# Performance work log

Measured on AMD Instinct MI355X. Metric: run time of the kernel, lower is better.

The kernel has to match this reference:

```python
import jax, jax.numpy as jnp
import numpy as np
from jax import lax


def _conv2d_same(x, w):
    # x: [B,Cin,H,W], w: [Cout,Cin,kh,kw], stride 1, SAME padding
    return lax.conv_general_dilated(x, w, (1, 1), 'SAME',
                                    dimension_numbers=('NCHW', 'OIHW', 'NCHW'))


def _descriptor(f_flat, w_a, b_a, w_aa, b_aa, w_m, b_m, w_mm, b_mm):
    # f_flat: [B,C,HW]; channel MLPs on avg/max pooled descriptors (1x1 convs == linear)
    avg = jnp.mean(f_flat, axis=-1)  # [B,C]
    mx = jnp.max(f_flat, axis=-1)    # [B,C]
    a = jax.nn.relu(avg @ w_a.T + b_a) @ w_aa.T + b_aa  # [B,C]
    m = jax.nn.relu(mx @ w_m.T + b_m) @ w_mm.T + b_mm   # [B,C]
    return a + m


def _spatial_gate(a_flat, b, c, h, w, conv1_w, conv1_b, conv2_w, conv2_b):
    a = a_flat.reshape(b, c, h, w)
    pooled = jnp.stack([jnp.mean(a, axis=1), jnp.max(a, axis=1)], axis=1)  # [B,2,H,W]
    y = jax.nn.relu(_conv2d_same(pooled, conv1_w) + conv1_b[None, :, None, None])
    y = _conv2d_same(y, conv2_w) + conv2_b[None, :, None, None]
    return jax.nn.softmax(y.reshape(b, 1, h * w), axis=-1)  # [B,1,HW]


def _cafm_forward(f1, f2,
                  w_avg1, b_avg1, w_max1, b_max1, w_avg11, b_avg11, w_max11, b_max11,
                  w_avg2, b_avg2, w_max2, b_max2, w_avg22, b_avg22, w_max22, b_max22,
                  conv1_w, conv1_b, conv2_w, conv2_b):
    b, c, h, w = f1.shape
    f1f = f1.reshape(b, c, h * w)
    f2f = f2.reshape(b, c, h * w)
    a1 = _descriptor(f1f, w_avg1, b_avg1, w_avg11, b_avg11, w_max1, b_max1, w_max11, b_max11)
    a2 = _descriptor(f2f, w_avg2, b_avg2, w_avg22, b_avg22, w_max2, b_max2, w_max22, b_max22)
    cross = jnp.einsum('bi,bj->bij', a1, a2)  # [B,C,C]
    at1 = jnp.einsum('bij,bjn->bin', jax.nn.softmax(cross, axis=-1), f1f)
    at2 = jnp.einsum('bij,bjn->bin', jax.nn.softmax(cross.transpose(0, 2, 1), axis=-1), f2f)
    g1 = _spatial_gate(at1, b, c, h, w, conv1_w, conv1_b, conv2_w, conv2_b)
    g2 = _spatial_gate(at2, b, c, h, w, conv1_w, conv1_b, conv2_w, conv2_b)
    o1 = (f1f * g1 + f1f).reshape(b, c, h, w)
    o2 = (f2f * g2 + f2f).reshape(b, c, h, w)
    return o1, o2


def setup_inputs() -> dict:
    key = jax.random.key(0)
    ks = jax.random.split(key, 24)
    B, C, H, W = 4, 64, 256, 256
    CR = 32  # reduction channels
    s = 0.05
    d = {
        'f1': jax.random.normal(ks[0], (B, C, H, W), jnp.float32),
        'f2': jax.random.normal(ks[1], (B, C, H, W), jnp.float32),
        'w_avg1': jax.random.normal(ks[2], (CR, C), jnp.float32) * s,
        'b_avg1': jnp.zeros((CR,), jnp.float32),
        'w_max1': jax.random.normal(ks[3], (CR, C), jnp.float32) * s,
        'b_max1': jnp.zeros((CR,), jnp.float32),
        'w_avg11': jax.random.normal(ks[4], (C, CR), jnp.float32) * s,
        'b_avg11': jnp.zeros((C,), jnp.float32),
        'w_max11': jax.random.normal(ks[5], (C, CR), jnp.float32) * s,
        'b_max11': jnp.zeros((C,), jnp.float32),
        'w_avg2': jax.random.normal(ks[6], (CR, C), jnp.float32) * s,
        'b_avg2': jnp.zeros((CR,), jnp.float32),
        'w_max2': jax.random.normal(ks[7], (CR, C), jnp.float32) * s,
        'b_max2': jnp.zeros((CR,), jnp.float32),
        'w_avg22': jax.random.normal(ks[8], (C, CR), jnp.float32) * s,
        'b_avg22': jnp.zeros((C,), jnp.float32),
        'w_max22': jax.random.normal(ks[9], (C, CR), jnp.float32) * s,
        'b_max22': jnp.zeros((C,), jnp.float32),
        'conv1_w': jax.random.normal(ks[10], (1, 2, 3, 3), jnp.float32) * s,
        'conv1_b': jnp.zeros((1,), jnp.float32),
        'conv2_w': jax.random.normal(ks[11], (1, 1, 3, 3), jnp.float32) * s,
        'conv2_b': jnp.zeros((1,), jnp.float32),
    }
    return d


def reference(f1, f2,
              w_avg1, b_avg1, w_max1, b_max1, w_avg11, b_avg11, w_max11, b_max11,
              w_avg2, b_avg2, w_max2, b_max2, w_avg22, b_avg22, w_max22, b_max22,
              conv1_w, conv1_b, conv2_w, conv2_b):
    return _cafm_forward(f1, f2,
                         w_avg1, b_avg1, w_max1, b_max1, w_avg11, b_avg11, w_max11, b_max11,
                         w_avg2, b_avg2, w_max2, b_max2, w_avg22, b_avg22, w_max22, b_max22,
                         conv1_w, conv1_b, conv2_w, conv2_b)
```

## Files before the change

### kernel.cpp

```cpp
#include <hip/hip_runtime.h>
#include <hip/hip_bf16.h>
#include <cstdint>

#define HW 65536

typedef __attribute__((ext_vector_type(8))) short bf16x8;
typedef __attribute__((ext_vector_type(4))) float f32x4;

#define OFF_RSUM 0
#define OFF_RMAX 512
#define OFF_PB   1024
#define OFF_POOL 33792
#define OFF_BM   33792
#define OFF_BS   35840
#define OFF_T1   1082368
#define OFF_Y    1606656
#define OFF_MX   2130944
#define OFF_IZ   2130952

__global__ __launch_bounds__(512) void k_reduce(const float* __restrict__ f1,
                                                const float* __restrict__ f2,
                                                float* __restrict__ ws) {
  int s = blockIdx.x;
  int t = s >> 8;
  const float* base = (t ? f2 : f1) + ((size_t)(s & 255) << 16);
  const float4* p4 = (const float4*)base;
  int tid = threadIdx.x;
  float sum = 0.f, mx = -3.4e38f;
#pragma unroll 8
  for (int it = 0; it < 32; ++it) {
    float4 v = p4[tid + (it << 9)];
    sum += (v.x + v.y) + (v.z + v.w);
    mx = fmaxf(mx, fmaxf(fmaxf(v.x, v.y), fmaxf(v.z, v.w)));
  }
  for (int o = 32; o > 0; o >>= 1) {
    sum += __shfl_down(sum, o);
    mx = fmaxf(mx, __shfl_down(mx, o));
  }
  __shared__ float ls[8], lm[8];
  int wid = tid >> 6, lane = tid & 63;
  if (lane == 0) { ls[wid] = sum; lm[wid] = mx; }
  __syncthreads();
  if (tid == 0) {
    float S = ls[0], M = lm[0];
    for (int w = 1; w < 8; ++w) { S += ls[w]; M = fmaxf(M, lm[w]); }
    ws[OFF_RSUM + s] = S;
    ws[OFF_RMAX + s] = M;
  }
}

__global__ __launch_bounds__(64) void k_mlp(
    const float* __restrict__ wsin, __hip_bfloat16* __restrict__ Pb,
    const float* __restrict__ w_avg1, const float* __restrict__ b_avg1,
    const float* __restrict__ w_max1, const float* __restrict__ b_max1,
    const float* __restrict__ w_avg11, const float* __restrict__ b_avg11,
    const float* __restrict__ w_max11, const float* __restrict__ b_max11,
    const float* __restrict__ w_avg2, const float* __restrict__ b_avg2,
    const float* __restrict__ w_max2, const float* __restrict__ b_max2,
    const float* __restrict__ w_avg22, const float* __restrict__ b_avg22,
    const float* __restrict__ w_max22, const float* __restrict__ b_max22) {
  int b = blockIdx.x, tid = threadIdx.x;
  __shared__ float avg1[64], mx1[64], avg2[64], mx2[64];
  __shared__ float ha1[32], hm1[32], ha2[32], hm2[32];
  __shared__ float a1[64], a2[64];
  avg1[tid] = wsin[OFF_RSUM + b * 64 + tid] * (1.f / 65536.f);
  mx1[tid]  = wsin[OFF_RMAX + b * 64 + tid];
  avg2[tid] = wsin[OFF_RSUM + 256 + b * 64 + tid] * (1.f / 65536.f);
  mx2[tid]  = wsin[OFF_RMAX + 256 + b * 64 + tid];
  __syncthreads();
  if (tid < 32) {
    float s1 = b_avg1[tid], s2 = b_max1[tid], s3 = b_avg2[tid], s4 = b_max2[tid];
    for (int c = 0; c < 64; ++c) {
      s1 += w_avg1[tid * 64 + c] * avg1[c];
      s2 += w_max1[tid * 64 + c] * mx1[c];
      s3 += w_avg2[tid * 64 + c] * avg2[c];
      s4 += w_max2[tid * 64 + c] * mx2[c];
    }
    ha1[tid] = fmaxf(s1, 0.f); hm1[tid] = fmaxf(s2, 0.f);
    ha2[tid] = fmaxf(s3, 0.f); hm2[tid] = fmaxf(s4, 0.f);
  }
  __syncthreads();
  {
    float s1 = b_avg11[tid] + b_max11[tid];
    float s2 = b_avg22[tid] + b_max22[tid];
    for (int k = 0; k < 32; ++k) {
      s1 += w_avg11[tid * 32 + k] * ha1[k] + w_max11[tid * 32 + k] * hm1[k];
      s2 += w_avg22[tid * 32 + k] * ha2[k] + w_max22[tid * 32 + k] * hm2[k];
    }
    a1[tid] = s1; a2[tid] = s2;
  }
  __syncthreads();
  {
    float s = a1[tid], m = -3.4e38f;
    for (int j = 0; j < 64; ++j) m = fmaxf(m, s * a2[j]);
    float sum = 0.f;
    for (int j = 0; j < 64; ++j) sum += __expf(s * a2[j] - m);
    float inv = 1.f / sum;
    __hip_bfloat16* row = Pb + (b << 12) + (tid << 6);
    for (int j = 0; j < 64; ++j)
      row[j] = __float2bfloat16(__expf(s * a2[j] - m) * inv);
  }
  {
    float s = a2[tid], m = -3.4e38f;
    for (int j = 0; j < 64; ++j) m = fmaxf(m, s * a1[j]);
    float sum = 0.f;
    for (int j = 0; j < 64; ++j) sum += __expf(s * a1[j] - m);
    float inv = 1.f / sum;
    __hip_bfloat16* row = Pb + ((4 + b) << 12) + (tid << 6);
    for (int j = 0; j < 64; ++j)
      row[j] = __float2bfloat16(__expf(s * a1[j] - m) * inv);
  }
}

__global__ __launch_bounds__(256) void k_pool(const float* __restrict__ f1,
                                              const float* __restrict__ f2,
                                              const __hip_bfloat16* __restrict__ Pall,
                                              float* __restrict__ pool) {
  int bx = blockIdx.x;
  int slice = bx >> 8;
  int t = slice >> 2;
  const float* f = (t ? f2 : f1) + ((size_t)(slice & 3) << 22);
  const __hip_bfloat16* P = Pall + (slice << 12);
  int wave = threadIdx.x >> 6, lane = threadIdx.x & 63;
  int c = lane & 15, q = lane >> 4;
  int n0 = ((bx & 255) << 8) + (wave << 6);

  bf16x8 A[4][2];
#pragma unroll
  for (int mt = 0; mt < 4; ++mt)
#pragma unroll
    for (int s = 0; s < 2; ++s)
      A[mt][s] = *(const bf16x8*)(P + ((mt * 16 + c) << 6) + s * 32 + q * 8);

  const float* fq = f + (size_t)(q * 8) * HW + n0 + c;
  float* poolp = pool + ((size_t)slice << 17);

#pragma unroll 2
  for (int nt = 0; nt < 4; ++nt) {
    int d = nt << 4;
    float bv0[8], bv1[8];
#pragma unroll
    for (int j = 0; j < 8; ++j) {
      bv0[j] = fq[(size_t)j * HW + d];
      bv1[j] = fq[(size_t)(j + 32) * HW + d];
    }
    union { bf16x8 v; __hip_bfloat162 h[4]; } u0, u1;
#pragma unroll
    for (int jj = 0; jj < 4; ++jj) {
      u0.h[jj] = __float22bfloat162_rn(make_float2(bv0[2 * jj], bv0[2 * jj + 1]));
      u1.h[jj] = __float22bfloat162_rn(make_float2(bv1[2 * jj], bv1[2 * jj + 1]));
    }
    f32x4 acc[4];
#pragma unroll
    for (int mt = 0; mt < 4; ++mt) {
      acc[mt] = (f32x4){0.f, 0.f, 0.f, 0.f};
      acc[mt] = __builtin_amdgcn_mfma_f32_16x16x32_bf16(A[mt][0], u0.v, acc[mt], 0, 0, 0);
      acc[mt] = __builtin_amdgcn_mfma_f32_16x16x32_bf16(A[mt][1], u1.v, acc[mt], 0, 0, 0);
    }
    float sum = 0.f, mxv = -3.4e38f;
#pragma unroll
    for (int mt = 0; mt < 4; ++mt)
#pragma unroll
      for (int r = 0; r < 4; ++r) {
        float v = acc[mt][r];
        sum += v;
        mxv = fmaxf(mxv, v);
      }
    sum += __shfl_xor(sum, 16);
    sum += __shfl_xor(sum, 32);
    mxv = fmaxf(mxv, __shfl_xor(mxv, 16));
    mxv = fmaxf(mxv, __shfl_xor(mxv, 32));
    int px = n0 + d + c;
    if (q == 0) poolp[px] = sum * (1.f / 64.f);
    if (q == 1) poolp[HW + px] = mxv;
  }
}

__global__ __launch_bounds__(256) void k_conv1(const float* __restrict__ pool,
                                               float* __restrict__ t1,
                                               const float* __restrict__ cw,
                                               const float* __restrict__ cb) {
  int idx = blockIdx.x * 256 + threadIdx.x;
  int t = idx >> 18;
  int rb = (idx >> 16) & 3;
  int n = idx & 65535;
  int h = n >> 8, w = n & 255;
  const float* pin = pool + ((size_t)((t << 2) | rb) << 17);
  float s = cb[0];
#pragma unroll
  for (int ci = 0; ci < 2; ++ci)
#pragma unroll
    for (int kh = -1; kh <= 1; ++kh)
#pragma unroll
      for (int kw = -1; kw <= 1; ++kw) {
        int hh = h + kh, ww = w + kw;
        if (hh >= 0 && hh < 256 && ww >= 0 && ww < 256)
          s += pin[ci * HW + (hh << 8) + ww] * cw[ci * 9 + (kh + 1) * 3 + (kw + 1)];
      }
  t1[((size_t)((t << 2) | rb) << 16) + n] = fmaxf(s, 0.f);
}

__global__ __launch_bounds__(256) void k_conv2(const float* __restrict__ t1,
                                               float* __restrict__ y,
                                               const float* __restrict__ cw,
                                               const float* __restrict__ cb,
                                               float* __restrict__ bm,
                                               float* __restrict__ bs) {
  int bx = blockIdx.x;
  int tid = threadIdx.x;
  int idx = bx * 256 + tid;
  int t = idx >> 18;
  int rb = (idx >> 16) & 3;
  int n = idx & 65535;
  int h = n >> 8, w = n & 255;
  const float* pin = t1 + ((size_t)((t << 2) | rb) << 16);
  float s = cb[0];
#pragma unroll
  for (int kh = -1; kh <= 1; ++kh)
#pragma unroll
    for (int kw = -1; kw <= 1; ++kw) {
      int hh = h + kh, ww = w + kw;
      if (hh >= 0 && hh < 256 && ww >= 0 && ww < 256)
        s += pin[(hh << 8) + ww] * cw[(kh + 1) * 3 + (kw + 1)];
    }
  y[((size_t)((t << 2) | rb) << 16) + n] = s;

  __shared__ float red[4];
  __shared__ float Mbs;
  float m = s;
  for (int o = 32; o > 0; o >>= 1) m = fmaxf(m, __shfl_xor(m, o));
  if ((tid & 63) == 0) red[tid >> 6] = m;
  __syncthreads();
  if (tid == 0) Mbs = fmaxf(fmaxf(red[0], red[1]), fmaxf(red[2], red[3]));
  __syncthreads();
  float Mb = Mbs;
  float z = __expf(s - Mb);
  for (int o = 32; o > 0; o >>= 1) z += __shfl_xor(z, o);
  if ((tid & 63) == 0) red[tid >> 6] = z;
  __syncthreads();
  if (tid == 0) {
    bm[bx] = Mb;
    bs[bx] = (red[0] + red[1]) + (red[2] + red[3]);
  }
}

__global__ __launch_bounds__(256) void k_comb(const float* __restrict__ bm,
                                              const float* __restrict__ bs,
                                              float* __restrict__ mx,
                                              float* __restrict__ iz) {
  int s = blockIdx.x;
  int tid = threadIdx.x;
  float m = bm[s * 256 + tid];
  float S = bs[s * 256 + tid];
  __shared__ float red[4];
  __shared__ float Msh;
  float mm = m;
  for (int o = 32; o > 0; o >>= 1) mm = fmaxf(mm, __shfl_xor(mm, o));
  if ((tid & 63) == 0) red[tid >> 6] = mm;
  __syncthreads();
  if (tid == 0) Msh = fmaxf(fmaxf(red[0], red[1]), fmaxf(red[2], red[3]));
  __syncthreads();
  float M = Msh;
  float z = __expf(m - M) * S;
  for (int o = 32; o > 0; o >>= 1) z += __shfl_xor(z, o);
  if ((tid & 63) == 0) red[tid >> 6] = z;
  __syncthreads();
  if (tid == 0) {
    mx[s] = M;
    iz[s] = 1.f / ((red[0] + red[1]) + (red[2] + red[3]));
  }
}

__global__ __launch_bounds__(256) void k_final(const float* __restrict__ f1,
                                               const float* __restrict__ f2,
                                               const float* __restrict__ y,
                                               const float* __restrict__ mx,
                                               const float* __restrict__ iz,
                                               float* __restrict__ out) {
  size_t idx = (size_t)blockIdx.x * 256 + threadIdx.x;
  size_t e = idx << 2;
  int t = (int)(e >> 24);
  int r = (int)(e & 16777215);
  int b = r >> 22;
  int n = r & 65535;
  int s = (t << 2) | b;
  float M = mx[s], Z = iz[s];
  float4 yv = *(const float4*)(y + ((size_t)s << 16) + n);
  float4 fv = *(const float4*)((t ? f2 : f1) + r);
  float4 o;
  o.x = fv.x * (1.f + __expf(yv.x - M) * Z);
  o.y = fv.y * (1.f + __expf(yv.y - M) * Z);
  o.z = fv.z * (1.f + __expf(yv.z - M) * Z);
  o.w = fv.w * (1.f + __expf(yv.w - M) * Z);
  *(float4*)(out + e) = o;
}

extern "C" void kernel_launch(void* const* d_in, const int* in_sizes, int n_in,
                              void* d_out, int out_size, void* d_ws, size_t ws_size,
                              hipStream_t stream) {
  const float* f1 = (const float*)d_in[0];
  const float* f2 = (const float*)d_in[1];
  const float* w_avg1  = (const float*)d_in[2];
  const float* b_avg1  = (const float*)d_in[3];
  const float* w_max1  = (const float*)d_in[4];
  const float* b_max1  = (const float*)d_in[5];
  const float* w_avg11 = (const float*)d_in[6];
  const float* b_avg11 = (const float*)d_in[7];
  const float* w_max11 = (const float*)d_in[8];
  const float* b_max11 = (const float*)d_in[9];
  const float* w_avg2  = (const float*)d_in[10];
  const float* b_avg2  = (const float*)d_in[11];
  const float* w_max2  = (const float*)d_in[12];
  const float* b_max2  = (const float*)d_in[13];
  const float* w_avg22 = (const float*)d_in[14];
  const float* b_avg22 = (const float*)d_in[15];
  const float* w_max22 = (const float*)d_in[16];
  const float* b_max22 = (const float*)d_in[17];
  const float* conv1_w = (const float*)d_in[18];
  const float* conv1_b = (const float*)d_in[19];
  const float* conv2_w = (const float*)d_in[20];
  const float* conv2_b = (const float*)d_in[21];
  float* ws = (float*)d_ws;
  float* out = (float*)d_out;
  __hip_bfloat16* Pb = (__hip_bfloat16*)(ws + OFF_PB);

  k_reduce<<<512, 512, 0, stream>>>(f1, f2, ws);
  k_mlp<<<4, 64, 0, stream>>>(ws, Pb,
                              w_avg1, b_avg1, w_max1, b_max1,
                              w_avg11, b_avg11, w_max11, b_max11,
                              w_avg2, b_avg2, w_max2, b_max2,
                              w_avg22, b_avg22, w_max22, b_max22);
  k_pool<<<2048, 256, 0, stream>>>(f1, f2, Pb, ws + OFF_POOL);
  k_conv1<<<2048, 256, 0, stream>>>(ws + OFF_POOL, ws + OFF_T1, conv1_w, conv1_b);
  k_conv2<<<2048, 256, 0, stream>>>(ws + OFF_T1, ws + OFF_Y, conv2_w, conv2_b,
                                    ws + OFF_BM, ws + OFF_BS);
  k_comb<<<8, 256, 0, stream>>>(ws + OFF_BM, ws + OFF_BS, ws + OFF_MX, ws + OFF_IZ);
  k_final<<<32768, 256, 0, stream>>>(f1, f2, ws + OFF_Y, ws + OFF_MX, ws + OFF_IZ, out);
}
```

Before: 339.4 us.

## Fuse reduce, MLP, pooling and convs into one persistent kernel with grid barriers

Replaces the six-kernel pipeline with a persistent mega-kernel of 1024 blocks that runs the reductions, channel MLP, softmax matrix build, MFMA pooling and both spatial convolutions. The phases are separated by atomic grid-wide barriers, and a small final kernel does the softmax normalization and output. The convolutions become tiled shared-memory stencils with halos, which drops the separate t1 buffer and one launch. Pooling now stages f into LDS as bf16 before the MFMA. This removes launch overhead and intermediate global traffic, at the cost of spin barriers that depend on all 1024 blocks being co-resident.

```diff
diff --git a/kernel.cpp b/kernel.cpp
--- a/kernel.cpp
+++ b/kernel.cpp
@@ -1,5 +1,4 @@
 #include <hip/hip_runtime.h>
-#include <hip/hip_bf16.h>
 #include <cstdint>
 
 #define HW 65536
@@ -7,50 +6,37 @@
 typedef __attribute__((ext_vector_type(8))) short bf16x8;
 typedef __attribute__((ext_vector_type(4))) float f32x4;
 
-#define OFF_RSUM 0
-#define OFF_RMAX 512
-#define OFF_PB   1024
-#define OFF_POOL 33792
-#define OFF_BM   33792
-#define OFF_BS   35840
-#define OFF_T1   1082368
-#define OFF_Y    1606656
-#define OFF_MX   2130944
-#define OFF_IZ   2130952
-
-__global__ __launch_bounds__(512) void k_reduce(const float* __restrict__ f1,
-                                                const float* __restrict__ f2,
-                                                float* __restrict__ ws) {
-  int s = blockIdx.x;
-  int t = s >> 8;
-  const float* base = (t ? f2 : f1) + ((size_t)(s & 255) << 16);
-  const float4* p4 = (const float4*)base;
-  int tid = threadIdx.x;
-  float sum = 0.f, mx = -3.4e38f;
-#pragma unroll 8
-  for (int it = 0; it < 32; ++it) {
-    float4 v = p4[tid + (it << 9)];
-    sum += (v.x + v.y) + (v.z + v.w);
-    mx = fmaxf(mx, fmaxf(fmaxf(v.x, v.y), fmaxf(v.z, v.w)));
-  }
-  for (int o = 32; o > 0; o >>= 1) {
-    sum += __shfl_down(sum, o);
-    mx = fmaxf(mx, __shfl_down(mx, o));
-  }
-  __shared__ float ls[8], lm[8];
-  int wid = tid >> 6, lane = tid & 63;
-  if (lane == 0) { ls[wid] = sum; lm[wid] = mx; }
-  __syncthreads();
-  if (tid == 0) {
-    float S = ls[0], M = lm[0];
-    for (int w = 1; w < 8; ++w) { S += ls[w]; M = fmaxf(M, lm[w]); }
-    ws[OFF_RSUM + s] = S;
-    ws[OFF_RMAX + s] = M;
-  }
-}
-
-__global__ __launch_bounds__(64) void k_mlp(
-    const float* __restrict__ wsin, __hip_bfloat16* __restrict__ Pb,
+#define OFF_CNT  0
+#define OFF_PS   16
+#define OFF_PM   1040
+#define OFF_A    2064
+#define OFF_PB   2576
+#define OFF_POOL 18960
+#define OFF_BM   1067536
+#define OFF_BS   1068560
+#define OFF_Y    1069584
+
+__device__ __forceinline__ unsigned short f2bf(float x) {
+  union { float f; unsigned u; } v; v.f = x;
+  unsigned r = v.u + 0x7fffu + ((v.u >> 16) & 1u);
+  return (unsigned short)(r >> 16);
+}
+
+__device__ __forceinline__ void gbar(unsigned* cnt, unsigned target) {
+  __syncthreads();
+  if (threadIdx.x == 0) {
+    __threadfence();
+    __hip_atomic_fetch_add(cnt, 1u, __ATOMIC_ACQ_REL, __HIP_MEMORY_SCOPE_AGENT);
+    while (__hip_atomic_load(cnt, __ATOMIC_ACQUIRE, __HIP_MEMORY_SCOPE_AGENT) < target)
+      __builtin_amdgcn_s_sleep(2);
+  }
+  __syncthreads();
+  __threadfence();
+}
+
+__global__ __launch_bounds__(256, 4) void k_mega(
+    const float* __restrict__ f1, const float* __restrict__ f2,
+    float* __restrict__ ws,
     const float* __restrict__ w_avg1, const float* __restrict__ b_avg1,
     const float* __restrict__ w_max1, const float* __restrict__ b_max1,
     const float* __restrict__ w_avg11, const float* __restrict__ b_avg11,
@@ -58,241 +44,263 @@
     const float* __restrict__ w_avg2, const float* __restrict__ b_avg2,
     const float* __restrict__ w_max2, const float* __restrict__ b_max2,
     const float* __restrict__ w_avg22, const float* __restrict__ b_avg22,
-    const float* __restrict__ w_max22, const float* __restrict__ b_max22) {
-  int b = blockIdx.x, tid = threadIdx.x;
-  __shared__ float avg1[64], mx1[64], avg2[64], mx2[64];
-  __shared__ float ha1[32], hm1[32], ha2[32], hm2[32];
-  __shared__ float a1[64], a2[64];
-  avg1[tid] = wsin[OFF_RSUM + b * 64 + tid] * (1.f / 65536.f);
-  mx1[tid]  = wsin[OFF_RMAX + b * 64 + tid];
-  avg2[tid] = wsin[OFF_RSUM + 256 + b * 64 + tid] * (1.f / 65536.f);
-  mx2[tid]  = wsin[OFF_RMAX + 256 + b * 64 + tid];
-  __syncthreads();
-  if (tid < 32) {
-    float s1 = b_avg1[tid], s2 = b_max1[tid], s3 = b_avg2[tid], s4 = b_max2[tid];
-    for (int c = 0; c < 64; ++c) {
-      s1 += w_avg1[tid * 64 + c] * avg1[c];
-      s2 += w_max1[tid * 64 + c] * mx1[c];
-      s3 += w_avg2[tid * 64 + c] * avg2[c];
-      s4 += w_max2[tid * 64 + c] * mx2[c];
-    }
-    ha1[tid] = fmaxf(s1, 0.f); hm1[tid] = fmaxf(s2, 0.f);
-    ha2[tid] = fmaxf(s3, 0.f); hm2[tid] = fmaxf(s4, 0.f);
-  }
-  __syncthreads();
+    const float* __restrict__ w_max22, const float* __restrict__ b_max22,
+    const float* __restrict__ cw1, const float* __restrict__ cb1,
+    const float* __restrict__ cw2, const float* __restrict__ cb2) {
+
+  __shared__ union {
+    unsigned short tile[64 * 258];
+    struct { float pl[2][20][36]; float t1l[18][34]; } cv;
+    struct { float avg1[64], mx1[64], avg2[64], mx2[64],
+             ha1[32], hm1[32], ha2[32], hm2[32]; } mlp;
+  } sm;
+  __shared__ float red[8];
+
+  unsigned* cnt = (unsigned*)ws;
+  const int tid = threadIdx.x;
+  const int bx  = blockIdx.x;
+  const int lane = tid & 63, wv = tid >> 6;
+
   {
-    float s1 = b_avg11[tid] + b_max11[tid];
-    float s2 = b_avg22[tid] + b_max22[tid];
-    for (int k = 0; k < 32; ++k) {
-      s1 += w_avg11[tid * 32 + k] * ha1[k] + w_max11[tid * 32 + k] * hm1[k];
-      s2 += w_avg22[tid * 32 + k] * ha2[k] + w_max22[tid * 32 + k] * hm2[k];
-    }
-    a1[tid] = s1; a2[tid] = s2;
-  }
-  __syncthreads();
+    int ss = bx >> 7, ch = (bx >> 1) & 63, half = bx & 1;
+    const float* fb = (ss >= 4) ? (f2 + ((size_t)(ss - 4) << 22))
+                                : (f1 + ((size_t)ss << 22));
+    const float4* p4 = (const float4*)(fb + (size_t)ch * HW + half * 32768);
+    float sum = 0.f, mx = -3.4e38f;
+#pragma unroll 8
+    for (int it = 0; it < 32; ++it) {
+      float4 v = p4[tid + (it << 8)];
+      sum += (v.x + v.y) + (v.z + v.w);
+      mx = fmaxf(mx, fmaxf(fmaxf(v.x, v.y), fmaxf(v.z, v.w)));
+    }
+    for (int o = 32; o > 0; o >>= 1) {
+      sum += __shfl_down(sum, o);
+      mx = fmaxf(mx, __shfl_down(mx, o));
+    }
+    if (lane == 0) { red[wv] = sum; red[4 + wv] = mx; }
+    __syncthreads();
+    if (tid == 0) {
+      ws[OFF_PS + bx] = red[0] + red[1] + red[2] + red[3];
+      ws[OFF_PM + bx] = fmaxf(fmaxf(red[4], red[5]), fmaxf(red[6], red[7]));
+    }
+  }
+  gbar(cnt + 0, 1024);
+
+  if (bx < 4) {
+    int b = bx;
+    if (tid < 64) {
+      int c = tid;
+      float s0 = ws[OFF_PS + b * 128 + c * 2] + ws[OFF_PS + b * 128 + c * 2 + 1];
+      sm.mlp.avg1[c] = s0 * (1.f / 65536.f);
+      sm.mlp.mx1[c] = fmaxf(ws[OFF_PM + b * 128 + c * 2], ws[OFF_PM + b * 128 + c * 2 + 1]);
+      float s2 = ws[OFF_PS + (4 + b) * 128 + c * 2] + ws[OFF_PS + (4 + b) * 128 + c * 2 + 1];
+      sm.mlp.avg2[c] = s2 * (1.f / 65536.f);
+      sm.mlp.mx2[c] = fmaxf(ws[OFF_PM + (4 + b) * 128 + c * 2], ws[OFF_PM + (4 + b) * 128 + c * 2 + 1]);
+    }
+    __syncthreads();
+    if (tid < 32) {
+      float s1 = b_avg1[tid], s2 = b_max1[tid], s3 = b_avg2[tid], s4 = b_max2[tid];
+      for (int c = 0; c < 64; ++c) {
+        s1 += w_avg1[tid * 64 + c] * sm.mlp.avg1[c];
+        s2 += w_max1[tid * 64 + c] * sm.mlp.mx1[c];
+        s3 += w_avg2[tid * 64 + c] * sm.mlp.avg2[c];
+        s4 += w_max2[tid * 64 + c] * sm.mlp.mx2[c];
+      }
+      sm.mlp.ha1[tid] = fmaxf(s1, 0.f); sm.mlp.hm1[tid] = fmaxf(s2, 0.f);
+      sm.mlp.ha2[tid] = fmaxf(s3, 0.f); sm.mlp.hm2[tid] = fmaxf(s4, 0.f);
+    }
+    __syncthreads();
+    if (tid < 64) {
+      float s1 = b_avg11[tid] + b_max11[tid];
+      float s2 = b_avg22[tid] + b_max22[tid];
+      for (int k = 0; k < 32; ++k) {
+        s1 += w_avg11[tid * 32 + k] * sm.mlp.ha1[k] + w_max11[tid * 32 + k] * sm.mlp.hm1[k];
+        s2 += w_avg22[tid * 32 + k] * sm.mlp.ha2[k] + w_max22[tid * 32 + k] * sm.mlp.hm2[k];
+      }
+      ws[OFF_A + b * 64 + tid] = s1;
+      ws[OFF_A + 256 + b * 64 + tid] = s2;
+    }
+  }
+  gbar(cnt + 1, 1024);
+
+  if (bx < 512) {
+    int ss = bx >> 6, i = bx & 63;
+    int t = ss >> 2, bb = ss & 3;
+    unsigned short* Pb = (unsigned short*)(ws + OFF_PB);
+    if (tid < 64) {
+      float sc = ws[OFF_A + (t ? 256 : 0) + bb * 64 + i];
+      float vj = ws[OFF_A + (t ? 0 : 256) + bb * 64 + tid];
+      float v = sc * vj;
+      float m = v;
+      for (int o = 32; o > 0; o >>= 1) m = fmaxf(m, __shfl_xor(m, o));
+      float e = __expf(v - m);
+      float s = e;
+      for (int o = 32; o > 0; o >>= 1) s += __shfl_xor(s, o);
+      Pb[(ss << 12) + (i << 6) + tid] = f2bf(e * (1.f / s));
+    }
+  }
+  gbar(cnt + 2, 1024);
+
   {
-    float s = a1[tid], m = -3.4e38f;
-    for (int j = 0; j < 64; ++j) m = fmaxf(m, s * a2[j]);
-    float sum = 0.f;
-    for (int j = 0; j < 64; ++j) sum += __expf(s * a2[j] - m);
-    float inv = 1.f / sum;
-    __hip_bfloat16* row = Pb + (b << 12) + (tid << 6);
-    for (int j = 0; j < 64; ++j)
-      row[j] = __float2bfloat16(__expf(s * a2[j] - m) * inv);
-  }
+    const int c = lane & 15, q = lane >> 4;
+    const unsigned short* Pb = (const unsigned short*)(ws + OFF_PB);
+    for (int u = bx; u < 2048; u += 1024) {
+      int ss = u >> 8, chunk = u & 255;
+      int n0 = chunk << 8;
+      const float* fb = (ss >= 4) ? (f2 + ((size_t)(ss - 4) << 22))
+                                  : (f1 + ((size_t)ss << 22));
+      __syncthreads();
+#pragma unroll 8
+      for (int i = 0; i < 64; ++i)
+        sm.tile[i * 258 + tid] = f2bf(fb[(size_t)i * HW + n0 + tid]);
+      __syncthreads();
+      bf16x8 A[4][2];
+#pragma unroll
+      for (int mt = 0; mt < 4; ++mt)
+#pragma unroll
+        for (int s = 0; s < 2; ++s)
+          A[mt][s] = *(const bf16x8*)(Pb + (ss << 12) + ((mt * 16 + c) << 6) + s * 32 + q * 8);
+      float* poolp = ws + OFF_POOL + (size_t)ss * (2 * HW);
+      int pxb = wv << 6;
+#pragma unroll
+      for (int nt = 0; nt < 4; ++nt) {
+        int pcol = pxb + (nt << 4) + c;
+        union { bf16x8 v; unsigned short s[8]; } u0, u1;
+#pragma unroll
+        for (int j = 0; j < 8; ++j) {
+          u0.s[j] = sm.tile[(q * 8 + j) * 258 + pcol];
+          u1.s[j] = sm.tile[(32 + q * 8 + j) * 258 + pcol];
+        }
+        f32x4 acc[4];
+#pragma unroll
+        for (int mt = 0; mt < 4; ++mt) {
+          acc[mt] = (f32x4){0.f, 0.f, 0.f, 0.f};
+          acc[mt] = __builtin_amdgcn_mfma_f32_16x16x32_bf16(A[mt][0], u0.v, acc[mt], 0, 0, 0);
+          acc[mt] = __builtin_amdgcn_mfma_f32_16x16x32_bf16(A[mt][1], u1.v, acc[mt], 0, 0, 0);
+        }
+        float sum = 0.f, mxv = -3.4e38f;
+#pragma unroll
+        for (int mt = 0; mt < 4; ++mt)
+#pragma unroll
+          for (int r = 0; r < 4; ++r) {
+            float v = acc[mt][r];
+            sum += v;
+            mxv = fmaxf(mxv, v);
+          }
+        sum += __shfl_xor(sum, 16);
+        sum += __shfl_xor(sum, 32);
+        mxv = fmaxf(mxv, __shfl_xor(mxv, 16));
+        mxv = fmaxf(mxv, __shfl_xor(mxv, 32));
+        int px = n0 + pcol;
+        if (q == 0) poolp[px] = sum * (1.f / 64.f);
+        if (q == 1) poolp[HW + px] = mxv;
+      }
+    }
+  }
+  gbar(cnt + 3, 1024);
+
   {
-    float s = a2[tid], m = -3.4e38f;
-    for (int j = 0; j < 64; ++j) m = fmaxf(m, s * a1[j]);
-    float sum = 0.f;
-    for (int j = 0; j < 64; ++j) sum += __expf(s * a1[j] - m);
-    float inv = 1.f / sum;
-    __hip_bfloat16* row = Pb + ((4 + b) << 12) + (tid << 6);
-    for (int j = 0; j < 64; ++j)
-      row[j] = __float2bfloat16(__expf(s * a1[j] - m) * inv);
-  }
-}
-
-__global__ __launch_bounds__(256) void k_pool(const float* __restrict__ f1,
-                                              const float* __restrict__ f2,
-                                              const __hip_bfloat16* __restrict__ Pall,
-                                              float* __restrict__ pool) {
-  int bx = blockIdx.x;
-  int slice = bx >> 8;
-  int t = slice >> 2;
-  const float* f = (t ? f2 : f1) + ((size_t)(slice & 3) << 22);
-  const __hip_bfloat16* P = Pall + (slice << 12);
-  int wave = threadIdx.x >> 6, lane = threadIdx.x & 63;
-  int c = lane & 15, q = lane >> 4;
-  int n0 = ((bx & 255) << 8) + (wave << 6);
-
-  bf16x8 A[4][2];
-#pragma unroll
-  for (int mt = 0; mt < 4; ++mt)
-#pragma unroll
-    for (int s = 0; s < 2; ++s)
-      A[mt][s] = *(const bf16x8*)(P + ((mt * 16 + c) << 6) + s * 32 + q * 8);
-
-  const float* fq = f + (size_t)(q * 8) * HW + n0 + c;
-  float* poolp = pool + ((size_t)slice << 17);
-
-#pragma unroll 2
-  for (int nt = 0; nt < 4; ++nt) {
-    int d = nt << 4;
-    float bv0[8], bv1[8];
-#pragma unroll
-    for (int j = 0; j < 8; ++j) {
-      bv0[j] = fq[(size_t)j * HW + d];
-      bv1[j] = fq[(size_t)(j + 32) * HW + d];
-    }
-    union { bf16x8 v; __hip_bfloat162 h[4]; } u0, u1;
-#pragma unroll
-    for (int jj = 0; jj < 4; ++jj) {
-      u0.h[jj] = __float22bfloat162_rn(make_float2(bv0[2 * jj], bv0[2 * jj + 1]));
-      u1.h[jj] = __float22bfloat162_rn(make_float2(bv1[2 * jj], bv1[2 * jj + 1]));
-    }
-    f32x4 acc[4];
-#pragma unroll
-    for (int mt = 0; mt < 4; ++mt) {
-      acc[mt] = (f32x4){0.f, 0.f, 0.f, 0.f};
-      acc[mt] = __builtin_amdgcn_mfma_f32_16x16x32_bf16(A[mt][0], u0.v, acc[mt], 0, 0, 0);
-      acc[mt] = __builtin_amdgcn_mfma_f32_16x16x32_bf16(A[mt][1], u1.v, acc[mt], 0, 0, 0);
-    }
-    float sum = 0.f, mxv = -3.4e38f;
-#pragma unroll
-    for (int mt = 0; mt < 4; ++mt)
-#pragma unroll
-      for (int r = 0; r < 4; ++r) {
-        float v = acc[mt][r];
-        sum += v;
-        mxv = fmaxf(mxv, v);
-      }
-    sum += __shfl_xor(sum, 16);
-    sum += __shfl_xor(sum, 32);
-    mxv = fmaxf(mxv, __shfl_xor(mxv, 16));
-    mxv = fmaxf(mxv, __shfl_xor(mxv, 32));
-    int px = n0 + d + c;
-    if (q == 0) poolp[px] = sum * (1.f / 64.f);
-    if (q == 1) poolp[HW + px] = mxv;
-  }
-}
-
-__global__ __launch_bounds__(256) void k_conv1(const float* __restrict__ pool,
-                                               float* __restrict__ t1,
-                                               const float* __restrict__ cw,
-                                               const float* __restrict__ cb) {
-  int idx = blockIdx.x * 256 + threadIdx.x;
-  int t = idx >> 18;
-  int rb = (idx >> 16) & 3;
-  int n = idx & 65535;
-  int h = n >> 8, w = n & 255;
-  const float* pin = pool + ((size_t)((t << 2) | rb) << 17);
-  float s = cb[0];
-#pragma unroll
-  for (int ci = 0; ci < 2; ++ci)
-#pragma unroll
-    for (int kh = -1; kh <= 1; ++kh)
-#pragma unroll
-      for (int kw = -1; kw <= 1; ++kw) {
-        int hh = h + kh, ww = w + kw;
-        if (hh >= 0 && hh < 256 && ww >= 0 && ww < 256)
-          s += pin[ci * HW + (hh << 8) + ww] * cw[ci * 9 + (kh + 1) * 3 + (kw + 1)];
-      }
-  t1[((size_t)((t << 2) | rb) << 16) + n] = fmaxf(s, 0.f);
-}
-
-__global__ __launch_bounds__(256) void k_conv2(const float* __restrict__ t1,
-                                               float* __restrict__ y,
-                                               const float* __restrict__ cw,
-                                               const float* __restrict__ cb,
-                                               float* __restrict__ bm,
-                                               float* __restrict__ bs) {
-  int bx = blockIdx.x;
-  int tid = threadIdx.x;
-  int idx = bx * 256 + tid;
-  int t = idx >> 18;
-  int rb = (idx >> 16) & 3;
-  int n = idx & 65535;
-  int h = n >> 8, w = n & 255;
-  const float* pin = t1 + ((size_t)((t << 2) | rb) << 16);
-  float s = cb[0];
-#pragma unroll
-  for (int kh = -1; kh <= 1; ++kh)
-#pragma unroll
-    for (int kw = -1; kw <= 1; ++kw) {
-      int hh = h + kh, ww = w + kw;
-      if (hh >= 0 && hh < 256 && ww >= 0 && ww < 256)
-        s += pin[(hh << 8) + ww] * cw[(kh + 1) * 3 + (kw + 1)];
-    }
-  y[((size_t)((t << 2) | rb) << 16) + n] = s;
-
-  __shared__ float red[4];
-  __shared__ float Mbs;
-  float m = s;
-  for (int o = 32; o > 0; o >>= 1) m = fmaxf(m, __shfl_xor(m, o));
-  if ((tid & 63) == 0) red[tid >> 6] = m;
-  __syncthreads();
-  if (tid == 0) Mbs = fmaxf(fmaxf(red[0], red[1]), fmaxf(red[2], red[3]));
-  __syncthreads();
-  float Mb = Mbs;
-  float z = __expf(s - Mb);
-  for (int o = 32; o > 0; o >>= 1) z += __shfl_xor(z, o);
-  if ((tid & 63) == 0) red[tid >> 6] = z;
-  __syncthreads();
-  if (tid == 0) {
-    bm[bx] = Mb;
-    bs[bx] = (red[0] + red[1]) + (red[2] + red[3]);
-  }
-}
-
-__global__ __launch_bounds__(256) void k_comb(const float* __restrict__ bm,
-                                              const float* __restrict__ bs,
-                                              float* __restrict__ mx,
-                                              float* __restrict__ iz) {
-  int s = blockIdx.x;
-  int tid = threadIdx.x;
-  float m = bm[s * 256 + tid];
-  float S = bs[s * 256 + tid];
-  __shared__ float red[4];
-  __shared__ float Msh;
-  float mm = m;
-  for (int o = 32; o > 0; o >>= 1) mm = fmaxf(mm, __shfl_xor(mm, o));
-  if ((tid & 63) == 0) red[tid >> 6] = mm;
-  __syncthreads();
-  if (tid == 0) Msh = fmaxf(fmaxf(red[0], red[1]), fmaxf(red[2], red[3]));
-  __syncthreads();
-  float M = Msh;
-  float z = __expf(m - M) * S;
-  for (int o = 32; o > 0; o >>= 1) z += __shfl_xor(z, o);
-  if ((tid & 63) == 0) red[tid >> 6] = z;
-  __syncthreads();
-  if (tid == 0) {
-    mx[s] = M;
-    iz[s] = 1.f / ((red[0] + red[1]) + (red[2] + red[3]));
+    int ss = bx >> 7, tile_id = bx & 127;
+    int h0 = (tile_id >> 3) << 4;
+    int w0 = (tile_id & 7) << 5;
+    const float* pp = ws + OFF_POOL + (size_t)ss * (2 * HW);
+    float c1b = cb1[0], c2b = cb2[0];
+    for (int i = tid; i < 1440; i += 256) {
+      int ch = (i >= 720), rem = i - ch * 720;
+      int rr = rem / 36, cc = rem - rr * 36;
+      int h = h0 - 2 + rr, w = w0 - 2 + cc;
+      float v = 0.f;
+      if (h >= 0 && h < 256 && w >= 0 && w < 256) v = pp[ch * HW + (h << 8) + w];
+      sm.cv.pl[ch][rr][cc] = v;
+    }
+    __syncthreads();
+    for (int i = tid; i < 612; i += 256) {
+      int rr = i / 34, cc = i - rr * 34;
+      int h = h0 - 1 + rr, w = w0 - 1 + cc;
+      float s = c1b;
+#pragma unroll
+      for (int ci = 0; ci < 2; ++ci)
+#pragma unroll
+        for (int kh = 0; kh < 3; ++kh)
+#pragma unroll
+          for (int kw = 0; kw < 3; ++kw)
+            s += sm.cv.pl[ci][rr + kh][cc + kw] * cw1[ci * 9 + kh * 3 + kw];
+      bool in = (h >= 0 && h < 256 && w >= 0 && w < 256);
+      sm.cv.t1l[rr][cc] = in ? fmaxf(s, 0.f) : 0.f;
+    }
+    __syncthreads();
+    float myy[2];
+    float m = -3.4e38f;
+#pragma unroll
+    for (int k2 = 0; k2 < 2; ++k2) {
+      int i = tid + (k2 << 8);
+      int rr = i >> 5, cc = i & 31;
+      float s = c2b;
+#pragma unroll
+      for (int kh = 0; kh < 3; ++kh)
+#pragma unroll
+        for (int kw = 0; kw < 3; ++kw)
+          s += sm.cv.t1l[rr + kh][cc + kw] * cw2[kh * 3 + kw];
+      ws[OFF_Y + (ss << 16) + ((h0 + rr) << 8) + w0 + cc] = s;
+      myy[k2] = s;
+      m = fmaxf(m, s);
+    }
+    for (int o = 32; o > 0; o >>= 1) m = fmaxf(m, __shfl_xor(m, o));
+    if (lane == 0) red[wv] = m;
+    __syncthreads();
+    float Mb = fmaxf(fmaxf(red[0], red[1]), fmaxf(red[2], red[3]));
+    float z = __expf(myy[0] - Mb) + __expf(myy[1] - Mb);
+    for (int o = 32; o > 0; o >>= 1) z += __shfl_xor(z, o);
+    if (lane == 0) red[4 + wv] = z;
+    __syncthreads();
+    if (tid == 0) {
+      ws[OFF_BM + bx] = Mb;
+      ws[OFF_BS + bx] = red[4] + red[5] + red[6] + red[7];
+    }
   }
 }
 
 __global__ __launch_bounds__(256) void k_final(const float* __restrict__ f1,
                                                const float* __restrict__ f2,
-                                               const float* __restrict__ y,
-                                               const float* __restrict__ mx,
-                                               const float* __restrict__ iz,
+                                               const float* __restrict__ ws,
                                                float* __restrict__ out) {
-  size_t idx = (size_t)blockIdx.x * 256 + threadIdx.x;
-  size_t e = idx << 2;
-  int t = (int)(e >> 24);
-  int r = (int)(e & 16777215);
-  int b = r >> 22;
-  int n = r & 65535;
-  int s = (t << 2) | b;
-  float M = mx[s], Z = iz[s];
-  float4 yv = *(const float4*)(y + ((size_t)s << 16) + n);
-  float4 fv = *(const float4*)((t ? f2 : f1) + r);
-  float4 o;
-  o.x = fv.x * (1.f + __expf(yv.x - M) * Z);
-  o.y = fv.y * (1.f + __expf(yv.y - M) * Z);
-  o.z = fv.z * (1.f + __expf(yv.z - M) * Z);
-  o.w = fv.w * (1.f + __expf(yv.w - M) * Z);
-  *(float4*)(out + e) = o;
+  int tid = threadIdx.x, bx = blockIdx.x;
+  int lane = tid & 63, wv = tid >> 6;
+  int s = bx >> 10;
+  __shared__ float red[8];
+  __shared__ float sIZ;
+  const float* bm = ws + OFF_BM + s * 128;
+  const float* bs = ws + OFF_BS + s * 128;
+  float m = (tid < 128) ? bm[tid] : -3.4e38f;
+  for (int o = 32; o > 0; o >>= 1) m = fmaxf(m, __shfl_xor(m, o));
+  if (lane == 0) red[wv] = m;
+  __syncthreads();
+  float M = fmaxf(fmaxf(red[0], red[1]), fmaxf(red[2], red[3]));
+  float z = (tid < 128) ? __expf(bm[tid] - M) * bs[tid] : 0.f;
+  for (int o = 32; o > 0; o >>= 1) z += __shfl_xor(z, o);
+  if (lane == 0) red[4 + wv] = z;
+  __syncthreads();
+  if (tid == 0) sIZ = 1.f / (red[4] + red[5] + red[6] + red[7]);
+  __syncthreads();
+  float iZ = sIZ;
+
+  const float* fsl = (s >= 4) ? (f2 + ((size_t)(s - 4) << 22))
+                              : (f1 + ((size_t)s << 22));
+  const float* ysl = ws + OFF_Y + (s << 16);
+  float* osl = out + ((size_t)s << 22);
+  int rbase = (bx & 1023) << 12;
+#pragma unroll
+  for (int ii = 0; ii < 4; ++ii) {
+    int r = rbase + tid * 16 + ii * 4;
+    float4 yv = *(const float4*)(ysl + (r & 65535));
+    float4 fv = *(const float4*)(fsl + r);
+    float4 o;
+    o.x = fv.x * (1.f + __expf(yv.x - M) * iZ);
+    o.y = fv.y * (1.f + __expf(yv.y - M) * iZ);
+    o.z = fv.z * (1.f + __expf(yv.z - M) * iZ);
+    o.w = fv.w * (1.f + __expf(yv.w - M) * iZ);
+    *(float4*)(osl + r) = o;
+  }
 }
 
 extern "C" void kernel_launch(void* const* d_in, const int* in_sizes, int n_in,
@@ -322,18 +330,13 @@
   const float* conv2_b = (const float*)d_in[21];
   float* ws = (float*)d_ws;
   float* out = (float*)d_out;
-  __hip_bfloat16* Pb = (__hip_bfloat16*)(ws + OFF_PB);
-
-  k_reduce<<<512, 512, 0, stream>>>(f1, f2, ws);
-  k_mlp<<<4, 64, 0, stream>>>(ws, Pb,
-                              w_avg1, b_avg1, w_max1, b_max1,
-                              w_avg11, b_avg11, w_max11, b_max11,
-                              w_avg2, b_avg2, w_max2, b_max2,
-                              w_avg22, b_avg22, w_max22, b_max22);
-  k_pool<<<2048, 256, 0, stream>>>(f1, f2, Pb, ws + OFF_POOL);
-  k_conv1<<<2048, 256, 0, stream>>>(ws + OFF_POOL, ws + OFF_T1, conv1_w, conv1_b);
-  k_conv2<<<2048, 256, 0, stream>>>(ws + OFF_T1, ws + OFF_Y, conv2_w, conv2_b,
-                                    ws + OFF_BM, ws + OFF_BS);
-  k_comb<<<8, 256, 0, stream>>>(ws + OFF_BM, ws + OFF_BS, ws + OFF_MX, ws + OFF_IZ);
-  k_final<<<32768, 256, 0, stream>>>(f1, f2, ws + OFF_Y, ws + OFF_MX, ws + OFF_IZ, out);
-}
+
+  hipMemsetAsync(d_ws, 0, 16, stream);
+  k_mega<<<1024, 256, 0, stream>>>(f1, f2, ws,
+                                   w_avg1, b_avg1, w_max1, b_max1,
+                                   w_avg11, b_avg11, w_max11, b_max11,
+                                   w_avg2, b_avg2, w_max2, b_max2,
+                                   w_avg22, b_avg22, w_max22, b_max22,
+                                   conv1_w, conv1_b, conv2_w, conv2_b);
+  k_final<<<8192, 256, 0, stream>>>(f1, f2, ws, out);
+}
```

New measurement: 1.072 ms. 216% more time.
